# Kernel optimization log

Measured on AMD Instinct MI355X. Metric: run time of the kernel, lower is better.

The kernel has to match this reference:

```python
import jax, jax.numpy as jnp
import numpy as np

B, C, H, W, S = 32, 512, 32, 32, 4
HW = H * W
OUT = HW // S  # conv1/conv2 out channels = 256
EPS = 1e-5


def setup_inputs() -> dict:
    key = jax.random.key(0)
    ks = jax.random.split(key, 8)
    d = {}
    d["x"] = jax.random.normal(ks[0], (B, C, H, W), jnp.float32)
    # conv1 / bn1 (operate on x_flat with 'channels' = h*w)
    d["w1"] = jax.random.normal(ks[1], (OUT, HW), jnp.float32) * 0.02
    d["b1"] = jnp.zeros((OUT,), jnp.float32)
    d["g1"] = jnp.ones((OUT,), jnp.float32)
    d["be1"] = jnp.zeros((OUT,), jnp.float32)
    d["m1"] = jax.random.normal(ks[2], (OUT,), jnp.float32) * 0.01
    d["v1"] = jnp.ones((OUT,), jnp.float32)
    # conv2 / bn2
    d["w2"] = jax.random.normal(ks[3], (OUT, HW), jnp.float32) * 0.02
    d["b2"] = jnp.zeros((OUT,), jnp.float32)
    d["g2"] = jnp.ones((OUT,), jnp.float32)
    d["be2"] = jnp.zeros((OUT,), jnp.float32)
    d["m2"] = jax.random.normal(ks[4], (OUT,), jnp.float32) * 0.01
    d["v2"] = jnp.ones((OUT,), jnp.float32)
    # conv3 / bn3 (1x1 conv on the real channel dim c)
    d["w3"] = jax.random.normal(ks[5], (C, C), jnp.float32) * 0.02
    d["b3"] = jnp.zeros((C,), jnp.float32)
    d["g3"] = jnp.ones((C,), jnp.float32)
    d["be3"] = jnp.zeros((C,), jnp.float32)
    d["m3"] = jax.random.normal(ks[6], (C,), jnp.float32) * 0.01
    d["v3"] = jnp.ones((C,), jnp.float32)
    # conv4: 1x1 conv mapping 1+2c channels -> 1
    d["w4"] = jax.random.normal(ks[7], (1 + 2 * C,), jnp.float32) * 0.02
    d["b4"] = jnp.zeros((), jnp.float32)
    return d


def _bn1d(t, g, be, m, v):
    # t: [b, o, c]; BatchNorm (eval mode) over channel axis 1
    scale = g / jnp.sqrt(v + EPS)
    return (t - m[:, None]) * scale[:, None] + be[:, None]


def reference(x, w1, b1, g1, be1, m1, v1,
              w2, b2, g2, be2, m2, v2,
              w3, b3, g3, be3, m3, v3,
              w4, b4):
    b, c, h, w = x.shape
    # x_flat: [b, h*w, c] -- conv1/conv2 are 1x1 convs over 'channels' = h*w
    xf = x.reshape(b, c, h * w).transpose(0, 2, 1)
    theta = jax.nn.relu(_bn1d(jnp.einsum('oq,bqc->boc', w1, xf) + b1[:, None],
                              g1, be1, m1, v1))  # [b, OUT, c]
    phi = jax.nn.relu(_bn1d(jnp.einsum('oq,bqc->boc', w2, xf) + b2[:, None],
                            g2, be2, m2, v2))    # [b, OUT, c]
    # per-batch conv2d-as-matmul loop collapses to one batched GEMM:
    # affinity[b, i, j] = sum_k phi[b, k, i] * theta[b, k, j]
    aff = jnp.einsum('bki,bkj->bij', phi, theta)  # [b, c, c]
    # x_embed: 1x1 conv + BN + ReLU + global average pool -> [b, c]
    scale3 = g3 / jnp.sqrt(v3 + EPS)
    xe = jnp.einsum('oc,bchw->bohw', w3, x) + b3[:, None, None]
    xe = jax.nn.relu((xe - m3[:, None, None]) * scale3[:, None, None]
                     + be3[:, None, None])
    xe = xe.mean(axis=(2, 3))  # [b, c]
    # conv4 over y = cat([x_embed, affinity_a, affinity_b], dim=1):
    # affinity_a[b,i,0,p] = aff[b,i,p]; affinity_b[b,i,0,p] = aff[b,p,i]
    logits = (w4[0] * xe
              + jnp.einsum('i,bip->bp', w4[1:1 + c], aff)
              + jnp.einsum('i,bpi->bp', w4[1 + c:], aff)
              + b4)
    a = jax.nn.sigmoid(logits)  # [b, c]
    return x * a[:, :, None, None]
```

## Files before the change

kernel.cpp:

```cpp
#include <hip/hip_runtime.h>
#include <math.h>

#define BB   32
#define CC   512
#define HWW  1024
#define OUTC 256
#define EPSV 1e-5f

typedef __attribute__((ext_vector_type(8))) short bfrag;
typedef __attribute__((ext_vector_type(4))) float f32x4;

__device__ inline unsigned short f2bf(float x){
  unsigned int uu = __float_as_uint(x);
  uu += 0x7fff + ((uu >> 16) & 1);
  return (unsigned short)(uu >> 16);
}
__device__ inline float bf2f(unsigned short h){
  return __uint_as_float(((unsigned int)h) << 16);
}

#define ASYNC16(g, l) \
  __builtin_amdgcn_global_load_lds((const __attribute__((address_space(1))) unsigned int*)(g), \
                                   (__attribute__((address_space(3))) unsigned int*)(l), 16, 0, 0)


__global__ __launch_bounds__(256) void prep(
    const float* __restrict__ x,
    const float* __restrict__ w1, const float* __restrict__ w2,
    const float* __restrict__ w3,
    unsigned short* __restrict__ Xhi, unsigned short* __restrict__ Xlo,
    unsigned short* __restrict__ XThi,
    unsigned short* __restrict__ Whi, unsigned short* __restrict__ Wlo,
    unsigned short* __restrict__ W3hi)
{
  if (blockIdx.z == 32) {
    int worker = (blockIdx.y * 16 + blockIdx.x) * 256 + threadIdx.x;
    for (int i = worker; i < 786432; i += 32768) {
      if (i < 524288) {
        float v = (i < 262144) ? w1[i] : w2[i - 262144];
        unsigned short h = f2bf(v);
        Whi[i] = h;
        Wlo[i] = f2bf(v - bf2f(h));
      } else {
        int j = i - 524288;
        W3hi[j] = f2bf(w3[j]);
      }
    }
    return;
  }
  __shared__ float T[64][65];
  const int b = blockIdx.z, c0 = blockIdx.y * 64, p0 = blockIdx.x * 64;
  const int tid = threadIdx.x, tr = tid >> 4, tc4 = (tid & 15) * 4;
  const float* xb = x + (size_t)b * 512 * 1024;
#pragma unroll
  for (int r = 0; r < 4; ++r) {
    int c = c0 + tr + r * 16;
    float4 v = *(const float4*)(xb + (size_t)c * 1024 + p0 + tc4);
    T[tr + r * 16][tc4 + 0] = v.x; T[tr + r * 16][tc4 + 1] = v.y;
    T[tr + r * 16][tc4 + 2] = v.z; T[tr + r * 16][tc4 + 3] = v.w;
    ushort4 h, l;
    h.x = f2bf(v.x); l.x = f2bf(v.x - bf2f(h.x));
    h.y = f2bf(v.y); l.y = f2bf(v.y - bf2f(h.y));
    h.z = f2bf(v.z); l.z = f2bf(v.z - bf2f(h.z));
    h.w = f2bf(v.w); l.w = f2bf(v.w - bf2f(h.w));
    size_t idx = (size_t)b * 524288 + (size_t)c * 1024 + p0 + tc4;
    *(ushort4*)(Xhi + idx) = h;
    *(ushort4*)(Xlo + idx) = l;
  }
  __syncthreads();
#pragma unroll
  for (int r = 0; r < 4; ++r) {
    int pl = tr + r * 16;
    ushort4 h;
    h.x = f2bf(T[tc4 + 0][pl]); h.y = f2bf(T[tc4 + 1][pl]);
    h.z = f2bf(T[tc4 + 2][pl]); h.w = f2bf(T[tc4 + 3][pl]);
    *(ushort4*)(XThi + (size_t)b * 524288 + (size_t)(p0 + pl) * 512 + c0 + tc4) = h;
  }
}

__global__ __launch_bounds__(256) void g1_mfma(
    const unsigned short* __restrict__ Xhi, const unsigned short* __restrict__ Xlo,
    const unsigned short* __restrict__ Whi, const unsigned short* __restrict__ Wlo,
    const float* __restrict__ b1p, const float* __restrict__ g1p,
    const float* __restrict__ be1p, const float* __restrict__ m1p, const float* __restrict__ v1p,
    const float* __restrict__ b2p, const float* __restrict__ g2p,
    const float* __restrict__ be2p, const float* __restrict__ m2p, const float* __restrict__ v2p,
    const float* __restrict__ w4,
    float* __restrict__ P2, float* __restrict__ u, float* __restrict__ t)
{
  __shared__ unsigned short sAh[4096], sAl[4096], sBh[4096], sBl[4096];
  const int f    = blockIdx.x;
  const int xcd  = f & 7;
  const int n0   = ((f >> 3) & 3) * 128;
  const int g    = ((f >> 5) << 3) | xcd;
  const int b    = g >> 2;
  const int c0   = (g & 3) * 128;
  const int tid  = threadIdx.x;
  const int wave = tid >> 6, lane = tid & 63;
  const int lr = lane >> 2;
  const int lcs = ((lane & 3) ^ (lr & 3)) * 8;
  const int wm = wave & 1, wn = wave >> 1;
  const int fr = lane & 15, fq = lane >> 4;
  const int fsw = (fq ^ (fr & 3)) * 8;

  const unsigned short* gb; unsigned short* lb;
  if (wave == 0)      { gb = Xhi + (size_t)b * 524288 + (size_t)c0 * 1024; lb = sAh; }
  else if (wave == 1) { gb = Xlo + (size_t)b * 524288 + (size_t)c0 * 1024; lb = sAl; }
  else if (wave == 2) { gb = Whi + (size_t)n0 * 1024; lb = sBh; }
  else                { gb = Wlo + (size_t)n0 * 1024; lb = sBl; }
  gb += (size_t)lr * 1024 + lcs;

  f32x4 acc[4][4];
  const f32x4 zz = {0.f, 0.f, 0.f, 0.f};
#pragma unroll
  for (int i = 0; i < 4; ++i)
#pragma unroll
    for (int j = 0; j < 4; ++j) acc[i][j] = zz;

  for (int kq = 0; kq < 1024; kq += 32) {
#pragma unroll
    for (int inst = 0; inst < 8; ++inst)
      ASYNC16(gb + (size_t)inst * 16 * 1024 + kq, lb + inst * 512);
    __syncthreads();
    bfrag ah[4], al[4], bh[4], bl[4];
#pragma unroll
    for (int i = 0; i < 4; ++i) {
      int off = (wm * 64 + i * 16 + fr) * 32 + fsw;
      ah[i] = *(const bfrag*)&sAh[off];
      al[i] = *(const bfrag*)&sAl[off];
    }
#pragma unroll
    for (int j = 0; j < 4; ++j) {
      int off = (wn * 64 + j * 16 + fr) * 32 + fsw;
      bh[j] = *(const bfrag*)&sBh[off];
      bl[j] = *(const bfrag*)&sBl[off];
    }
#pragma unroll
    for (int i = 0; i < 4; ++i)
#pragma unroll
      for (int j = 0; j < 4; ++j) {
        acc[i][j] = __builtin_amdgcn_mfma_f32_16x16x32_bf16(ah[i], bh[j], acc[i][j], 0, 0, 0);
        acc[i][j] = __builtin_amdgcn_mfma_f32_16x16x32_bf16(ah[i], bl[j], acc[i][j], 0, 0, 0);
        acc[i][j] = __builtin_amdgcn_mfma_f32_16x16x32_bf16(al[i], bh[j], acc[i][j], 0, 0, 0);
      }
    __syncthreads();
  }

  const float *bias, *gg, *bes, *mm, *vv_; int cof;
  if (n0 < 256) { bias = b1p; gg = g1p; bes = be1p; mm = m1p; vv_ = v1p; cof = 0; }
  else          { bias = b2p; gg = g2p; bes = be2p; mm = m2p; vv_ = v2p; cof = 256; }
  const float* wsel = (n0 < 256) ? (w4 + 513) : (w4 + 1);
  float* dsel = (n0 < 256) ? (t + b * 256) : (u + b * 256);
  const int cobase = ((n0 < 256) ? n0 : n0 - 256) + wn * 64;
  float wt[4][4];
#pragma unroll
  for (int i = 0; i < 4; ++i)
#pragma unroll
    for (int r = 0; r < 4; ++r)
      wt[i][r] = wsel[c0 + wm * 64 + i * 16 + fq * 4 + r];

#pragma unroll
  for (int j = 0; j < 4; ++j) {
    int co = n0 + wn * 64 + j * 16 + fr;
    int q = co - cof;
    float s  = gg[q] * rsqrtf(vv_[q] + EPSV);
    float sh = (bias[q] - mm[q]) * s + bes[q];
    float psum = 0.f;
#pragma unroll
    for (int i = 0; i < 4; ++i) {
      int crow = c0 + wm * 64 + i * 16 + fq * 4;
      float* dst = P2 + ((size_t)b * 512 + crow) * 512 + co;
#pragma unroll
      for (int r = 0; r < 4; ++r) {
        float val = fmaxf(acc[i][j][r] * s + sh, 0.f);
        dst[(size_t)r * 512] = val;
        psum += wt[i][r] * val;
      }
    }
    psum += __shfl_xor(psum, 16);
    psum += __shfl_xor(psum, 32);
    if (fq == 0) atomicAdd(&dsel[cobase + j * 16 + fr], psum);
  }
}

__global__ __launch_bounds__(256) void g2_mfma(
    const unsigned short* __restrict__ W3hi, const unsigned short* __restrict__ XThi,
    const float* __restrict__ b3p, const float* __restrict__ g3p,
    const float* __restrict__ be3p, const float* __restrict__ m3p, const float* __restrict__ v3p,
    float* __restrict__ xe_acc)
{
  __shared__ unsigned short sA[4096], sB[4096];
  const int b  = blockIdx.z;
  const int n0 = blockIdx.x * 128;
  const int m0 = blockIdx.y * 128;
  const int tid = threadIdx.x;
  const int wave = tid >> 6, lane = tid & 63;
  const int lr = lane >> 2;
  const int lcs = ((lane & 3) ^ (lr & 3)) * 8;
  const int wm = wave & 1, wn = wave >> 1;
  const int fr = lane & 15, fq = lane >> 4;
  const int fsw = (fq ^ (fr & 3)) * 8;

  const unsigned short* gb; unsigned short* lb;
  if (wave < 2) { gb = W3hi + (size_t)(m0 + wave * 64) * 512; lb = sA + wave * 2048; }
  else { gb = XThi + (size_t)b * 524288 + (size_t)(n0 + (wave - 2) * 64) * 512; lb = sB + (wave - 2) * 2048; }
  gb += (size_t)lr * 512 + lcs;

  f32x4 acc[4][4];
  const f32x4 zz = {0.f, 0.f, 0.f, 0.f};
#pragma unroll
  for (int i = 0; i < 4; ++i)
#pragma unroll
    for (int j = 0; j < 4; ++j) acc[i][j] = zz;

  for (int kq = 0; kq < 512; kq += 32) {
#pragma unroll
    for (int inst = 0; inst < 4; ++inst)
      ASYNC16(gb + (size_t)inst * 16 * 512 + kq, lb + inst * 512);
    __syncthreads();
    bfrag af[4], bf[4];
#pragma unroll
    for (int i = 0; i < 4; ++i)
      af[i] = *(const bfrag*)&sA[(wm * 64 + i * 16 + fr) * 32 + fsw];
#pragma unroll
    for (int j = 0; j < 4; ++j)
      bf[j] = *(const bfrag*)&sB[(wn * 64 + j * 16 + fr) * 32 + fsw];
#pragma unroll
    for (int i = 0; i < 4; ++i)
#pragma unroll
      for (int j = 0; j < 4; ++j)
        acc[i][j] = __builtin_amdgcn_mfma_f32_16x16x32_bf16(af[i], bf[j], acc[i][j], 0, 0, 0);
    __syncthreads();
  }

#pragma unroll
  for (int i = 0; i < 4; ++i) {
#pragma unroll
    for (int r = 0; r < 4; ++r) {
      int o = m0 + wm * 64 + i * 16 + fq * 4 + r;
      float s  = g3p[o] * rsqrtf(v3p[o] + EPSV);
      float sh = (b3p[o] - m3p[o]) * s + be3p[o];
      float v = fmaxf(acc[i][0][r] * s + sh, 0.f) + fmaxf(acc[i][1][r] * s + sh, 0.f)
              + fmaxf(acc[i][2][r] * s + sh, 0.f) + fmaxf(acc[i][3][r] * s + sh, 0.f);
      v += __shfl_xor(v, 1); v += __shfl_xor(v, 2);
      v += __shfl_xor(v, 4); v += __shfl_xor(v, 8);
      if (fr == 0) atomicAdd(&xe_acc[b * 512 + o], v);
    }
  }
}

__global__ __launch_bounds__(256) void k4_gate_out(
    const float* __restrict__ P2, const float* __restrict__ u,
    const float* __restrict__ t, const float* __restrict__ xe_acc,
    const float* __restrict__ w4, const float* __restrict__ b4,
    const float* __restrict__ x, float* __restrict__ out)
{
  __shared__ float us[256], ts[256];
  const int b = blockIdx.x;
  us[threadIdx.x] = u[b * 256 + threadIdx.x];
  ts[threadIdx.x] = t[b * 256 + threadIdx.x];
  __syncthreads();
  const int wave = threadIdx.x >> 6, lane = threadIdx.x & 63;
  const int p = blockIdx.y * 4 + wave;
  const float* row = P2 + ((size_t)b * 512 + p) * 512;
  float4 th = *(const float4*)&row[lane * 4];
  float4 ph = *(const float4*)&row[256 + lane * 4];
  int ki = lane * 4;
  float rs = th.x * us[ki] + th.y * us[ki + 1] + th.z * us[ki + 2] + th.w * us[ki + 3]
           + ph.x * ts[ki] + ph.y * ts[ki + 1] + ph.z * ts[ki + 2] + ph.w * ts[ki + 3];
  rs += __shfl_xor(rs, 1);  rs += __shfl_xor(rs, 2);  rs += __shfl_xor(rs, 4);
  rs += __shfl_xor(rs, 8);  rs += __shfl_xor(rs, 16); rs += __shfl_xor(rs, 32);
  float xe = xe_acc[b * 512 + p] * (1.f / 1024.f);
  float logit = w4[0] * xe + rs + b4[0];
  float a = 1.f / (1.f + expf(-logit));
  const float4* xr = (const float4*)(x + ((size_t)b * 512 + p) * 1024);
  float4* orow = (float4*)(out + ((size_t)b * 512 + p) * 1024);
#pragma unroll
  for (int r2 = 0; r2 < 4; ++r2) {
    float4 xv = xr[lane + r2 * 64];
    float4 ov; ov.x = xv.x * a; ov.y = xv.y * a; ov.z = xv.z * a; ov.w = xv.w * a;
    orow[lane + r2 * 64] = ov;
  }
}

__global__ __launch_bounds__(256) void k1_theta_phi(
    const float* __restrict__ x,
    const float* __restrict__ w1, const float* __restrict__ b1,
    const float* __restrict__ g1, const float* __restrict__ be1,
    const float* __restrict__ m1, const float* __restrict__ v1,
    const float* __restrict__ w2, const float* __restrict__ b2,
    const float* __restrict__ g2, const float* __restrict__ be2,
    const float* __restrict__ m2, const float* __restrict__ v2,
    float* __restrict__ P)
{
  __shared__ __align__(16) float Ws[32][68];
  __shared__ __align__(16) float Xs[32][68];
  const int b  = blockIdx.z;
  const int o0 = blockIdx.y * 64;
  const int c0 = blockIdx.x * 64;
  const int tid = threadIdx.x;
  const int tx = tid & 15, ty = tid >> 4;
  const float* __restrict__ Wbase = (o0 < OUTC) ? (w1 + (size_t)o0 * HWW)
                                                : (w2 + (size_t)(o0 - OUTC) * HWW);
  const float* __restrict__ xb = x + (size_t)b * CC * HWW;
  float acc[4][4] = {{0.f}};
  for (int k0 = 0; k0 < HWW; k0 += 32) {
#pragma unroll
    for (int r = 0; r < 2; ++r) {
      int id  = tid + (r << 8);
      int row = id >> 3;
      int cg  = (id & 7) << 2;
      float4 wv = *(const float4*)(Wbase + (size_t)row * HWW + k0 + cg);
      Ws[cg+0][row] = wv.x; Ws[cg+1][row] = wv.y; Ws[cg+2][row] = wv.z; Ws[cg+3][row] = wv.w;
      float4 xv = *(const float4*)(xb + (size_t)(c0 + row) * HWW + k0 + cg);
      Xs[cg+0][row] = xv.x; Xs[cg+1][row] = xv.y; Xs[cg+2][row] = xv.z; Xs[cg+3][row] = xv.w;
    }
    __syncthreads();
#pragma unroll
    for (int k = 0; k < 32; ++k) {
      float4 av = *(const float4*)&Ws[k][ty * 4];
      float4 bv = *(const float4*)&Xs[k][tx * 4];
      acc[0][0] += av.x*bv.x; acc[0][1] += av.x*bv.y; acc[0][2] += av.x*bv.z; acc[0][3] += av.x*bv.w;
      acc[1][0] += av.y*bv.x; acc[1][1] += av.y*bv.y; acc[1][2] += av.y*bv.z; acc[1][3] += av.y*bv.w;
      acc[2][0] += av.z*bv.x; acc[2][1] += av.z*bv.y; acc[2][2] += av.z*bv.z; acc[2][3] += av.z*bv.w;
      acc[3][0] += av.w*bv.x; acc[3][1] += av.w*bv.y; acc[3][2] += av.w*bv.z; acc[3][3] += av.w*bv.w;
    }
    __syncthreads();
  }
  const float *bias, *g, *be, *m, *v; int ob;
  if (o0 < OUTC) { bias = b1; g = g1; be = be1; m = m1; v = v1; ob = o0; }
  else           { bias = b2; g = g2; be = be2; m = m2; v = v2; ob = o0 - OUTC; }
#pragma unroll
  for (int i = 0; i < 4; ++i) {
    int oi = ob + ty * 4 + i;
    float sc = g[oi] * rsqrtf(v[oi] + EPSV);
    float sh = be[oi] - m[oi] * sc;
    float bb = bias[oi];
    float4 ov;
    ov.x = fmaxf((acc[i][0] + bb) * sc + sh, 0.f);
    ov.y = fmaxf((acc[i][1] + bb) * sc + sh, 0.f);
    ov.z = fmaxf((acc[i][2] + bb) * sc + sh, 0.f);
    ov.w = fmaxf((acc[i][3] + bb) * sc + sh, 0.f);
    int oo = o0 + ty * 4 + i;
    *(float4*)(P + ((size_t)b * 512 + oo) * 512 + c0 + tx * 4) = ov;
  }
}

__global__ __launch_bounds__(256) void k2_xe(
    const float* __restrict__ x, const float* __restrict__ w3,
    const float* __restrict__ b3, const float* __restrict__ g3,
    const float* __restrict__ be3, const float* __restrict__ m3,
    const float* __restrict__ v3, float* __restrict__ xe_acc)
{
  __shared__ __align__(16) float As[32][68];
  __shared__ __align__(16) float Bs[32][68];
  const int b  = blockIdx.z;
  const int o0 = blockIdx.y * 64;
  const int p0 = blockIdx.x * 64;
  const int tid = threadIdx.x;
  const int tx = tid & 15, ty = tid >> 4;
  const float* __restrict__ xb = x + (size_t)b * CC * HWW;
  float acc[4][4] = {{0.f}};
  for (int ck = 0; ck < CC; ck += 32) {
#pragma unroll
// ... 59 lines not shown
  for (int off = 32; off > 0; off >>= 1) {
    su += __shfl_down(su, off);
    st += __shfl_down(st, off);
  }
  if (lane == 0) { u[b * OUTC + k] = su; t[b * OUTC + k] = st; }
}

__global__ __launch_bounds__(256) void k4_gate(
    const float* __restrict__ P, const float* __restrict__ u,
    const float* __restrict__ t, const float* __restrict__ xe_acc,
    const float* __restrict__ w4, const float* __restrict__ b4,
    float* __restrict__ amul)
{
  __shared__ float us[256], ts[256];
  const int b = blockIdx.x;
  const int p = blockIdx.y * 256 + threadIdx.x;
  us[threadIdx.x] = u[b * OUTC + threadIdx.x];
  ts[threadIdx.x] = t[b * OUTC + threadIdx.x];
  __syncthreads();
  const float* __restrict__ theta = P + (size_t)b * 512 * 512;
  const float* __restrict__ phi   = theta + 256 * 512;
  float r = 0.f, s = 0.f;
#pragma unroll 8
  for (int k = 0; k < OUTC; ++k) {
    r += us[k] * theta[(size_t)k * 512 + p];
    s += ts[k] * phi[(size_t)k * 512 + p];
  }
  float xe = xe_acc[b * CC + p] * (1.0f / 1024.0f);
  float logit = w4[0] * xe + r + s + b4[0];
  amul[b * CC + p] = 1.0f / (1.0f + expf(-logit));
}

__global__ __launch_bounds__(256) void k5_out(
    const float* __restrict__ x, const float* __restrict__ amul,
    float* __restrict__ out)
{
  int i = blockIdx.x * 256 + threadIdx.x;
  float4 xv = ((const float4*)x)[i];
  float a = amul[i >> 8];
  float4 ov; ov.x = xv.x * a; ov.y = xv.y * a; ov.z = xv.z * a; ov.w = xv.w * a;
  ((float4*)out)[i] = ov;
}

extern "C" void kernel_launch(void* const* d_in, const int* in_sizes, int n_in,
                              void* d_out, int out_size, void* d_ws, size_t ws_size,
                              hipStream_t stream)
{
  (void)in_sizes; (void)n_in; (void)out_size;
  const float* x   = (const float*)d_in[0];
  const float* w1  = (const float*)d_in[1];
  const float* b1  = (const float*)d_in[2];
  const float* g1  = (const float*)d_in[3];
  const float* be1 = (const float*)d_in[4];
  const float* m1  = (const float*)d_in[5];
  const float* v1  = (const float*)d_in[6];
  const float* w2  = (const float*)d_in[7];
  const float* b2  = (const float*)d_in[8];
  const float* g2  = (const float*)d_in[9];
  const float* be2 = (const float*)d_in[10];
  const float* m2  = (const float*)d_in[11];
  const float* v2  = (const float*)d_in[12];
  const float* w3  = (const float*)d_in[13];
  const float* b3  = (const float*)d_in[14];
  const float* g3  = (const float*)d_in[15];
  const float* be3 = (const float*)d_in[16];
  const float* m3  = (const float*)d_in[17];
  const float* v3  = (const float*)d_in[18];
  const float* w4  = (const float*)d_in[19];
  const float* b4  = (const float*)d_in[20];
  float* out = (float*)d_out;

  if (ws_size >= 136970240ull) {
    float* P2     = (float*)d_ws;
    float* xe_acc = P2 + 8388608;
    float* u      = P2 + 8404992;
    float* t      = P2 + 8413184;
    unsigned short* Xhi  = (unsigned short*)((char*)d_ws + 33685504);
    unsigned short* Xlo  = Xhi + 16777216;
    unsigned short* XThi = Xlo + 16777216;
    unsigned short* Whi  = XThi + 16777216;
    unsigned short* Wlo  = Whi + 524288;
    unsigned short* W3hi = Wlo + 524288;

    hipMemsetAsync(xe_acc, 0, 32768 * sizeof(float), stream);

    prep<<<dim3(16, 8, 33), 256, 0, stream>>>(x, w1, w2, w3, Xhi, Xlo, XThi,
                                              Whi, Wlo, W3hi);
    g1_mfma<<<dim3(512), 256, 0, stream>>>(Xhi, Xlo, Whi, Wlo,
        b1, g1, be1, m1, v1, b2, g2, be2, m2, v2, w4, P2, u, t);
    g2_mfma<<<dim3(8, 4, 32), 256, 0, stream>>>(W3hi, XThi, b3, g3, be3, m3, v3, xe_acc);
    k4_gate_out<<<dim3(32, 128), 256, 0, stream>>>(P2, u, t, xe_acc, w4, b4, x, out);
  } else {
    float* P      = (float*)d_ws;
    float* xe_acc = P + (size_t)BB * 512 * 512;
    float* u      = xe_acc + BB * CC;
    float* t      = u + BB * OUTC;
    float* amul   = t + BB * OUTC;

    hipMemsetAsync(xe_acc, 0, (size_t)BB * CC * sizeof(float), stream);

    dim3 blk(256);
    k1_theta_phi<<<dim3(8, 8, BB), blk, 0, stream>>>(x, w1, b1, g1, be1, m1, v1,
                                                     w2, b2, g2, be2, m2, v2, P);
    k2_xe<<<dim3(16, 8, BB), blk, 0, stream>>>(x, w3, b3, g3, be3, m3, v3, xe_acc);
    k3_ut<<<dim3(BB, 64), blk, 0, stream>>>(P, w4, u, t);
    k4_gate<<<dim3(BB, 2), blk, 0, stream>>>(P, u, t, xe_acc, w4, b4, amul);
    k5_out<<<dim3((BB * CC * HWW / 4) / 256), blk, 0, stream>>>(x, amul, out);
  }
}
```

Baseline: 291.8 us.

## Fuse both GEMM kernels into one launch and fold accumulator zeroing into prep

The theta/phi GEMM and the x_embed GEMM now run as two block ranges of a single kernel, so the two run concurrently instead of back to back. The theta/phi tile is narrowed from 128 to 64 output columns, which doubles its block count to fill more CUs. The separate memset of the xe/u/t accumulators is replaced by zeroing inside the prep kernel's weight-conversion blocks. In exchange, the narrower tiles reload the same X tiles from memory twice as often, and the shared-memory size is set by the larger of the two paths.

```diff
diff --git a/kernel.cpp b/kernel.cpp
--- a/kernel.cpp
+++ b/kernel.cpp
@@ -31,10 +31,12 @@
     unsigned short* __restrict__ Xhi, unsigned short* __restrict__ Xlo,
     unsigned short* __restrict__ XThi,
     unsigned short* __restrict__ Whi, unsigned short* __restrict__ Wlo,
-    unsigned short* __restrict__ W3hi)
+    unsigned short* __restrict__ W3hi,
+    float* __restrict__ accz)
 {
   if (blockIdx.z == 32) {
     int worker = (blockIdx.y * 16 + blockIdx.x) * 256 + threadIdx.x;
+    accz[worker] = 0.f;
     for (int i = worker; i < 786432; i += 32768) {
       if (i < 524288) {
         float v = (i < 262144) ? w1[i] : w2[i - 262144];
@@ -78,173 +80,170 @@
   }
 }
 
-__global__ __launch_bounds__(256) void g1_mfma(
+__global__ __launch_bounds__(256) void gemm_fused(
     const unsigned short* __restrict__ Xhi, const unsigned short* __restrict__ Xlo,
     const unsigned short* __restrict__ Whi, const unsigned short* __restrict__ Wlo,
+    const unsigned short* __restrict__ W3hi, const unsigned short* __restrict__ XThi,
     const float* __restrict__ b1p, const float* __restrict__ g1p,
     const float* __restrict__ be1p, const float* __restrict__ m1p, const float* __restrict__ v1p,
     const float* __restrict__ b2p, const float* __restrict__ g2p,
     const float* __restrict__ be2p, const float* __restrict__ m2p, const float* __restrict__ v2p,
+    const float* __restrict__ b3p, const float* __restrict__ g3p,
+    const float* __restrict__ be3p, const float* __restrict__ m3p, const float* __restrict__ v3p,
     const float* __restrict__ w4,
-    float* __restrict__ P2, float* __restrict__ u, float* __restrict__ t)
-{
-  __shared__ unsigned short sAh[4096], sAl[4096], sBh[4096], sBl[4096];
-  const int f    = blockIdx.x;
-  const int xcd  = f & 7;
-  const int n0   = ((f >> 3) & 3) * 128;
-  const int g    = ((f >> 5) << 3) | xcd;
-  const int b    = g >> 2;
-  const int c0   = (g & 3) * 128;
+    float* __restrict__ P2, float* __restrict__ u, float* __restrict__ t,
+    float* __restrict__ xe_acc)
+{
+  __shared__ unsigned short smem[12288];
+  const int fid  = blockIdx.x;
   const int tid  = threadIdx.x;
   const int wave = tid >> 6, lane = tid & 63;
   const int lr = lane >> 2;
   const int lcs = ((lane & 3) ^ (lr & 3)) * 8;
-  const int wm = wave & 1, wn = wave >> 1;
   const int fr = lane & 15, fq = lane >> 4;
   const int fsw = (fq ^ (fr & 3)) * 8;
 
-  const unsigned short* gb; unsigned short* lb;
-  if (wave == 0)      { gb = Xhi + (size_t)b * 524288 + (size_t)c0 * 1024; lb = sAh; }
-  else if (wave == 1) { gb = Xlo + (size_t)b * 524288 + (size_t)c0 * 1024; lb = sAl; }
-  else if (wave == 2) { gb = Whi + (size_t)n0 * 1024; lb = sBh; }
-  else                { gb = Wlo + (size_t)n0 * 1024; lb = sBl; }
-  gb += (size_t)lr * 1024 + lcs;
-
-  f32x4 acc[4][4];
-  const f32x4 zz = {0.f, 0.f, 0.f, 0.f};
-#pragma unroll
-  for (int i = 0; i < 4; ++i)
-#pragma unroll
-    for (int j = 0; j < 4; ++j) acc[i][j] = zz;
-
-  for (int kq = 0; kq < 1024; kq += 32) {
-#pragma unroll
-    for (int inst = 0; inst < 8; ++inst)
-      ASYNC16(gb + (size_t)inst * 16 * 1024 + kq, lb + inst * 512);
-    __syncthreads();
-    bfrag ah[4], al[4], bh[4], bl[4];
+  if (fid < 1024) {
+    unsigned short* sAh = smem;
+    unsigned short* sAl = smem + 4096;
+    unsigned short* sBh = smem + 8192;
+    unsigned short* sBl = smem + 10240;
+    const int xcd = fid & 7;
+    const int n0  = ((fid >> 3) & 7) * 64;
+    const int bc  = ((fid >> 6) << 3) | xcd;
+    const int b   = bc >> 2;
+    const int c0  = (bc & 3) * 128;
+    const int wm = wave & 1, wn = wave >> 1;
+
+    const unsigned short* gb; unsigned short* lb; int ninst;
+    if (wave == 0)      { gb = Xhi + (size_t)b * 524288 + (size_t)c0 * 1024; lb = sAh; ninst = 8; }
+    else if (wave == 1) { gb = Xlo + (size_t)b * 524288 + (size_t)c0 * 1024; lb = sAl; ninst = 8; }
+    else if (wave == 2) { gb = Whi + (size_t)n0 * 1024; lb = sBh; ninst = 4; }
+    else                { gb = Wlo + (size_t)n0 * 1024; lb = sBl; ninst = 4; }
+    gb += (size_t)lr * 1024 + lcs;
+
+    f32x4 acc[4][2];
+    const f32x4 zz = {0.f, 0.f, 0.f, 0.f};
+#pragma unroll
+    for (int i = 0; i < 4; ++i) { acc[i][0] = zz; acc[i][1] = zz; }
+
+    for (int kq = 0; kq < 1024; kq += 32) {
+      for (int inst = 0; inst < ninst; ++inst)
+        ASYNC16(gb + (size_t)inst * 16 * 1024 + kq, lb + inst * 512);
+      __syncthreads();
+      bfrag ah[4], al[4], bh[2], bl[2];
+#pragma unroll
+      for (int i = 0; i < 4; ++i) {
+        int off = (wm * 64 + i * 16 + fr) * 32 + fsw;
+        ah[i] = *(const bfrag*)&sAh[off];
+        al[i] = *(const bfrag*)&sAl[off];
+      }
+#pragma unroll
+      for (int j = 0; j < 2; ++j) {
+        int off = (wn * 32 + j * 16 + fr) * 32 + fsw;
+        bh[j] = *(const bfrag*)&sBh[off];
+        bl[j] = *(const bfrag*)&sBl[off];
+      }
+#pragma unroll
+      for (int i = 0; i < 4; ++i)
+#pragma unroll
+        for (int j = 0; j < 2; ++j) {
+          acc[i][j] = __builtin_amdgcn_mfma_f32_16x16x32_bf16(ah[i], bh[j], acc[i][j], 0, 0, 0);
+          acc[i][j] = __builtin_amdgcn_mfma_f32_16x16x32_bf16(ah[i], bl[j], acc[i][j], 0, 0, 0);
+          acc[i][j] = __builtin_amdgcn_mfma_f32_16x16x32_bf16(al[i], bh[j], acc[i][j], 0, 0, 0);
+        }
+      __syncthreads();
+    }
+
+    const float *bias, *gg, *bes, *mm, *vv_; int cof;
+    if (n0 < 256) { bias = b1p; gg = g1p; bes = be1p; mm = m1p; vv_ = v1p; cof = 0; }
+    else          { bias = b2p; gg = g2p; bes = be2p; mm = m2p; vv_ = v2p; cof = 256; }
+    const float* wsel = (n0 < 256) ? (w4 + 513) : (w4 + 1);
+    float* dsel = (n0 < 256) ? (t + b * 256) : (u + b * 256);
+    const int cobase = (n0 - cof) + wn * 32;
+    float wt[4][4];
+#pragma unroll
+    for (int i = 0; i < 4; ++i)
+#pragma unroll
+      for (int r = 0; r < 4; ++r)
+        wt[i][r] = wsel[c0 + wm * 64 + i * 16 + fq * 4 + r];
+
+#pragma unroll
+    for (int j = 0; j < 2; ++j) {
+      int co = n0 + wn * 32 + j * 16 + fr;
+      int q = co - cof;
+      float s  = gg[q] * rsqrtf(vv_[q] + EPSV);
+      float sh = (bias[q] - mm[q]) * s + bes[q];
+      float psum = 0.f;
+#pragma unroll
+      for (int i = 0; i < 4; ++i) {
+        int crow = c0 + wm * 64 + i * 16 + fq * 4;
+        float* dst = P2 + ((size_t)b * 512 + crow) * 512 + co;
+#pragma unroll
+        for (int r = 0; r < 4; ++r) {
+          float val = fmaxf(acc[i][j][r] * s + sh, 0.f);
+          dst[(size_t)r * 512] = val;
+          psum += wt[i][r] * val;
+        }
+      }
+      psum += __shfl_xor(psum, 16);
+      psum += __shfl_xor(psum, 32);
+      if (fq == 0) atomicAdd(&dsel[cobase + j * 16 + fr], psum);
+    }
+  } else {
+    unsigned short* sA = smem;
+    unsigned short* sB = smem + 4096;
+    const int h  = fid - 1024;
+    const int n0 = (h & 7) * 128;
+    const int m0 = ((h >> 3) & 3) * 128;
+    const int b  = h >> 5;
+    const int wm = wave & 1, wn = wave >> 1;
+
+    const unsigned short* gb; unsigned short* lb;
+    if (wave < 2) { gb = W3hi + (size_t)(m0 + wave * 64) * 512; lb = sA + wave * 2048; }
+    else { gb = XThi + (size_t)b * 524288 + (size_t)(n0 + (wave - 2) * 64) * 512; lb = sB + (wave - 2) * 2048; }
+    gb += (size_t)lr * 512 + lcs;
+
+    f32x4 acc[4][4];
+    const f32x4 zz = {0.f, 0.f, 0.f, 0.f};
+#pragma unroll
+    for (int i = 0; i < 4; ++i)
+#pragma unroll
+      for (int j = 0; j < 4; ++j) acc[i][j] = zz;
+
+    for (int kq = 0; kq < 512; kq += 32) {
+#pragma unroll
+      for (int inst = 0; inst < 4; ++inst)
+        ASYNC16(gb + (size_t)inst * 16 * 512 + kq, lb + inst * 512);
+      __syncthreads();
+      bfrag af[4], bf[4];
+#pragma unroll
+      for (int i = 0; i < 4; ++i)
+        af[i] = *(const bfrag*)&sA[(wm * 64 + i * 16 + fr) * 32 + fsw];
+#pragma unroll
+      for (int j = 0; j < 4; ++j)
+        bf[j] = *(const bfrag*)&sB[(wn * 64 + j * 16 + fr) * 32 + fsw];
+#pragma unroll
+      for (int i = 0; i < 4; ++i)
+#pragma unroll
+        for (int j = 0; j < 4; ++j)
+          acc[i][j] = __builtin_amdgcn_mfma_f32_16x16x32_bf16(af[i], bf[j], acc[i][j], 0, 0, 0);
+      __syncthreads();
+    }
+
 #pragma unroll
     for (int i = 0; i < 4; ++i) {
-      int off = (wm * 64 + i * 16 + fr) * 32 + fsw;
-      ah[i] = *(const bfrag*)&sAh[off];
-      al[i] = *(const bfrag*)&sAl[off];
-    }
-#pragma unroll
-    for (int j = 0; j < 4; ++j) {
-      int off = (wn * 64 + j * 16 + fr) * 32 + fsw;
-      bh[j] = *(const bfrag*)&sBh[off];
-      bl[j] = *(const bfrag*)&sBl[off];
-    }
-#pragma unroll
-    for (int i = 0; i < 4; ++i)
-#pragma unroll
-      for (int j = 0; j < 4; ++j) {
-        acc[i][j] = __builtin_amdgcn_mfma_f32_16x16x32_bf16(ah[i], bh[j], acc[i][j], 0, 0, 0);
-        acc[i][j] = __builtin_amdgcn_mfma_f32_16x16x32_bf16(ah[i], bl[j], acc[i][j], 0, 0, 0);
-        acc[i][j] = __builtin_amdgcn_mfma_f32_16x16x32_bf16(al[i], bh[j], acc[i][j], 0, 0, 0);
+#pragma unroll
+      for (int r = 0; r < 4; ++r) {
+        int o = m0 + wm * 64 + i * 16 + fq * 4 + r;
+        float s  = g3p[o] * rsqrtf(v3p[o] + EPSV);
+        float sh = (b3p[o] - m3p[o]) * s + be3p[o];
+        float v = fmaxf(acc[i][0][r] * s + sh, 0.f) + fmaxf(acc[i][1][r] * s + sh, 0.f)
+                + fmaxf(acc[i][2][r] * s + sh, 0.f) + fmaxf(acc[i][3][r] * s + sh, 0.f);
+        v += __shfl_xor(v, 1); v += __shfl_xor(v, 2);
+        v += __shfl_xor(v, 4); v += __shfl_xor(v, 8);
+        if (fr == 0) atomicAdd(&xe_acc[b * 512 + o], v);
       }
-    __syncthreads();
-  }
-
-  const float *bias, *gg, *bes, *mm, *vv_; int cof;
-  if (n0 < 256) { bias = b1p; gg = g1p; bes = be1p; mm = m1p; vv_ = v1p; cof = 0; }
-  else          { bias = b2p; gg = g2p; bes = be2p; mm = m2p; vv_ = v2p; cof = 256; }
-  const float* wsel = (n0 < 256) ? (w4 + 513) : (w4 + 1);
-  float* dsel = (n0 < 256) ? (t + b * 256) : (u + b * 256);
-  const int cobase = ((n0 < 256) ? n0 : n0 - 256) + wn * 64;
-  float wt[4][4];
-#pragma unroll
-  for (int i = 0; i < 4; ++i)
-#pragma unroll
-    for (int r = 0; r < 4; ++r)
-      wt[i][r] = wsel[c0 + wm * 64 + i * 16 + fq * 4 + r];
-
-#pragma unroll
-  for (int j = 0; j < 4; ++j) {
-    int co = n0 + wn * 64 + j * 16 + fr;
-    int q = co - cof;
-    float s  = gg[q] * rsqrtf(vv_[q] + EPSV);
-    float sh = (bias[q] - mm[q]) * s + bes[q];
-    float psum = 0.f;
-#pragma unroll
-    for (int i = 0; i < 4; ++i) {
-      int crow = c0 + wm * 64 + i * 16 + fq * 4;
-      float* dst = P2 + ((size_t)b * 512 + crow) * 512 + co;
-#pragma unroll
-      for (int r = 0; r < 4; ++r) {
-        float val = fmaxf(acc[i][j][r] * s + sh, 0.f);
-        dst[(size_t)r * 512] = val;
-        psum += wt[i][r] * val;
-      }
-    }
-    psum += __shfl_xor(psum, 16);
-    psum += __shfl_xor(psum, 32);
-    if (fq == 0) atomicAdd(&dsel[cobase + j * 16 + fr], psum);
-  }
-}
-
-__global__ __launch_bounds__(256) void g2_mfma(
-    const unsigned short* __restrict__ W3hi, const unsigned short* __restrict__ XThi,
-    const float* __restrict__ b3p, const float* __restrict__ g3p,
-    const float* __restrict__ be3p, const float* __restrict__ m3p, const float* __restrict__ v3p,
-    float* __restrict__ xe_acc)
-{
-  __shared__ unsigned short sA[4096], sB[4096];
-  const int b  = blockIdx.z;
-  const int n0 = blockIdx.x * 128;
-  const int m0 = blockIdx.y * 128;
-  const int tid = threadIdx.x;
-  const int wave = tid >> 6, lane = tid & 63;
-  const int lr = lane >> 2;
-  const int lcs = ((lane & 3) ^ (lr & 3)) * 8;
-  const int wm = wave & 1, wn = wave >> 1;
-  const int fr = lane & 15, fq = lane >> 4;
-  const int fsw = (fq ^ (fr & 3)) * 8;
-
-  const unsigned short* gb; unsigned short* lb;
-  if (wave < 2) { gb = W3hi + (size_t)(m0 + wave * 64) * 512; lb = sA + wave * 2048; }
-  else { gb = XThi + (size_t)b * 524288 + (size_t)(n0 + (wave - 2) * 64) * 512; lb = sB + (wave - 2) * 2048; }
-  gb += (size_t)lr * 512 + lcs;
-
-  f32x4 acc[4][4];
-  const f32x4 zz = {0.f, 0.f, 0.f, 0.f};
-#pragma unroll
-  for (int i = 0; i < 4; ++i)
-#pragma unroll
-    for (int j = 0; j < 4; ++j) acc[i][j] = zz;
-
-  for (int kq = 0; kq < 512; kq += 32) {
-#pragma unroll
-    for (int inst = 0; inst < 4; ++inst)
-      ASYNC16(gb + (size_t)inst * 16 * 512 + kq, lb + inst * 512);
-    __syncthreads();
-    bfrag af[4], bf[4];
-#pragma unroll
-    for (int i = 0; i < 4; ++i)
-      af[i] = *(const bfrag*)&sA[(wm * 64 + i * 16 + fr) * 32 + fsw];
-#pragma unroll
-    for (int j = 0; j < 4; ++j)
-      bf[j] = *(const bfrag*)&sB[(wn * 64 + j * 16 + fr) * 32 + fsw];
-#pragma unroll
-    for (int i = 0; i < 4; ++i)
-#pragma unroll
-      for (int j = 0; j < 4; ++j)
-        acc[i][j] = __builtin_amdgcn_mfma_f32_16x16x32_bf16(af[i], bf[j], acc[i][j], 0, 0, 0);
-    __syncthreads();
-  }
-
-#pragma unroll
-  for (int i = 0; i < 4; ++i) {
-#pragma unroll
-    for (int r = 0; r < 4; ++r) {
-      int o = m0 + wm * 64 + i * 16 + fq * 4 + r;
-      float s  = g3p[o] * rsqrtf(v3p[o] + EPSV);
-      float sh = (b3p[o] - m3p[o]) * s + be3p[o];
-      float v = fmaxf(acc[i][0][r] * s + sh, 0.f) + fmaxf(acc[i][1][r] * s + sh, 0.f)
-              + fmaxf(acc[i][2][r] * s + sh, 0.f) + fmaxf(acc[i][3][r] * s + sh, 0.f);
-      v += __shfl_xor(v, 1); v += __shfl_xor(v, 2);
-      v += __shfl_xor(v, 4); v += __shfl_xor(v, 8);
-      if (fr == 0) atomicAdd(&xe_acc[b * 512 + o], v);
     }
   }
 }
@@ -505,13 +504,11 @@
     unsigned short* Wlo  = Whi + 524288;
     unsigned short* W3hi = Wlo + 524288;
 
-    hipMemsetAsync(xe_acc, 0, 32768 * sizeof(float), stream);
-
     prep<<<dim3(16, 8, 33), 256, 0, stream>>>(x, w1, w2, w3, Xhi, Xlo, XThi,
-                                              Whi, Wlo, W3hi);
-    g1_mfma<<<dim3(512), 256, 0, stream>>>(Xhi, Xlo, Whi, Wlo,
-        b1, g1, be1, m1, v1, b2, g2, be2, m2, v2, w4, P2, u, t);
-    g2_mfma<<<dim3(8, 4, 32), 256, 0, stream>>>(W3hi, XThi, b3, g3, be3, m3, v3, xe_acc);
+                                              Whi, Wlo, W3hi, xe_acc);
+    gemm_fused<<<dim3(2048), 256, 0, stream>>>(Xhi, Xlo, Whi, Wlo, W3hi, XThi,
+        b1, g1, be1, m1, v1, b2, g2, be2, m2, v2, b3, g3, be3, m3, v3,
+        w4, P2, u, t, xe_acc);
     k4_gate_out<<<dim3(32, 128), 256, 0, stream>>>(P2, u, t, xe_acc, w4, b4, x, out);
   } else {
     float* P      = (float*)d_ws;
```

Measured after the change: 289.1 us. Within noise of the previous version (-0.9%).

## Merge conv1/conv2 and conv3 GEMMs into one interleaved launch, drop memset

Applied to the files above, without the earlier changes.

The two MFMA GEMM kernels become one launch whose blocks are interleaved, one theta/phi tile for every two x_embed tiles, so both GEMMs can share the GPU at once and the tail of the first no longer idles it. Zeroing of the xe_acc/u/t accumulators moves from a separate memset into the weight-conversion blocks of prep, removing one stream operation. The gate/output kernel now handles four channel rows per wave with a quarter of the blocks. In exchange, every block of the fused kernel reserves the larger 32KB shared buffer, which can lower occupancy for the conv3 tiles.

```diff
diff --git a/kernel.cpp b/kernel.cpp
--- a/kernel.cpp
+++ b/kernel.cpp
@@ -31,10 +31,12 @@
     unsigned short* __restrict__ Xhi, unsigned short* __restrict__ Xlo,
     unsigned short* __restrict__ XThi,
     unsigned short* __restrict__ Whi, unsigned short* __restrict__ Wlo,
-    unsigned short* __restrict__ W3hi)
+    unsigned short* __restrict__ W3hi,
+    float* __restrict__ accz)
 {
   if (blockIdx.z == 32) {
     int worker = (blockIdx.y * 16 + blockIdx.x) * 256 + threadIdx.x;
+    accz[worker] = 0.f;
     for (int i = worker; i < 786432; i += 32768) {
       if (i < 524288) {
         float v = (i < 262144) ? w1[i] : w2[i - 262144];
@@ -78,23 +80,22 @@
   }
 }
 
-__global__ __launch_bounds__(256) void g1_mfma(
+__global__ __launch_bounds__(256) void gemm_fused(
     const unsigned short* __restrict__ Xhi, const unsigned short* __restrict__ Xlo,
     const unsigned short* __restrict__ Whi, const unsigned short* __restrict__ Wlo,
+    const unsigned short* __restrict__ W3hi, const unsigned short* __restrict__ XThi,
     const float* __restrict__ b1p, const float* __restrict__ g1p,
     const float* __restrict__ be1p, const float* __restrict__ m1p, const float* __restrict__ v1p,
     const float* __restrict__ b2p, const float* __restrict__ g2p,
     const float* __restrict__ be2p, const float* __restrict__ m2p, const float* __restrict__ v2p,
+    const float* __restrict__ b3p, const float* __restrict__ g3p,
+    const float* __restrict__ be3p, const float* __restrict__ m3p, const float* __restrict__ v3p,
     const float* __restrict__ w4,
-    float* __restrict__ P2, float* __restrict__ u, float* __restrict__ t)
-{
-  __shared__ unsigned short sAh[4096], sAl[4096], sBh[4096], sBl[4096];
-  const int f    = blockIdx.x;
-  const int xcd  = f & 7;
-  const int n0   = ((f >> 3) & 3) * 128;
-  const int g    = ((f >> 5) << 3) | xcd;
-  const int b    = g >> 2;
-  const int c0   = (g & 3) * 128;
+    float* __restrict__ P2, float* __restrict__ u, float* __restrict__ t,
+    float* __restrict__ xe_acc)
+{
+  __shared__ unsigned short smem[16384];
+  const int fid  = blockIdx.x;
   const int tid  = threadIdx.x;
   const int wave = tid >> 6, lane = tid & 63;
   const int lr = lane >> 2;
@@ -103,148 +104,149 @@
   const int fr = lane & 15, fq = lane >> 4;
   const int fsw = (fq ^ (fr & 3)) * 8;
 
-  const unsigned short* gb; unsigned short* lb;
-  if (wave == 0)      { gb = Xhi + (size_t)b * 524288 + (size_t)c0 * 1024; lb = sAh; }
-  else if (wave == 1) { gb = Xlo + (size_t)b * 524288 + (size_t)c0 * 1024; lb = sAl; }
-  else if (wave == 2) { gb = Whi + (size_t)n0 * 1024; lb = sBh; }
-  else                { gb = Wlo + (size_t)n0 * 1024; lb = sBl; }
-  gb += (size_t)lr * 1024 + lcs;
-
-  f32x4 acc[4][4];
-  const f32x4 zz = {0.f, 0.f, 0.f, 0.f};
-#pragma unroll
-  for (int i = 0; i < 4; ++i)
-#pragma unroll
-    for (int j = 0; j < 4; ++j) acc[i][j] = zz;
-
-  for (int kq = 0; kq < 1024; kq += 32) {
-#pragma unroll
-    for (int inst = 0; inst < 8; ++inst)
-      ASYNC16(gb + (size_t)inst * 16 * 1024 + kq, lb + inst * 512);
-    __syncthreads();
-    bfrag ah[4], al[4], bh[4], bl[4];
+  if (fid % 3 == 0) {
+    unsigned short* sAh = smem;
+    unsigned short* sAl = smem + 4096;
+    unsigned short* sBh = smem + 8192;
+    unsigned short* sBl = smem + 12288;
+    const int m  = fid / 3;
+    const int n0 = (m >> 7) * 128;
+    const int g  = m & 127;
+    const int b  = g >> 2;
+    const int c0 = (g & 3) * 128;
+
+    const unsigned short* gb; unsigned short* lb;
+    if (wave == 0)      { gb = Xhi + (size_t)b * 524288 + (size_t)c0 * 1024; lb = sAh; }
+    else if (wave == 1) { gb = Xlo + (size_t)b * 524288 + (size_t)c0 * 1024; lb = sAl; }
+    else if (wave == 2) { gb = Whi + (size_t)n0 * 1024; lb = sBh; }
+    else                { gb = Wlo + (size_t)n0 * 1024; lb = sBl; }
+    gb += (size_t)lr * 1024 + lcs;
+
+    f32x4 acc[4][4];
+    const f32x4 zz = {0.f, 0.f, 0.f, 0.f};
+#pragma unroll
+    for (int i = 0; i < 4; ++i)
+#pragma unroll
+      for (int j = 0; j < 4; ++j) acc[i][j] = zz;
+
+    for (int kq = 0; kq < 1024; kq += 32) {
+#pragma unroll
+      for (int inst = 0; inst < 8; ++inst)
+        ASYNC16(gb + (size_t)inst * 16 * 1024 + kq, lb + inst * 512);
+      __syncthreads();
+      bfrag ah[4], al[4], bh[4], bl[4];
+#pragma unroll
+      for (int i = 0; i < 4; ++i) {
+        int off = (wm * 64 + i * 16 + fr) * 32 + fsw;
+        ah[i] = *(const bfrag*)&sAh[off];
+        al[i] = *(const bfrag*)&sAl[off];
+      }
+#pragma unroll
+      for (int j = 0; j < 4; ++j) {
+        int off = (wn * 64 + j * 16 + fr) * 32 + fsw;
+        bh[j] = *(const bfrag*)&sBh[off];
+        bl[j] = *(const bfrag*)&sBl[off];
+      }
+#pragma unroll
+      for (int i = 0; i < 4; ++i)
+#pragma unroll
+        for (int j = 0; j < 4; ++j) {
+          acc[i][j] = __builtin_amdgcn_mfma_f32_16x16x32_bf16(ah[i], bh[j], acc[i][j], 0, 0, 0);
+          acc[i][j] = __builtin_amdgcn_mfma_f32_16x16x32_bf16(ah[i], bl[j], acc[i][j], 0, 0, 0);
+          acc[i][j] = __builtin_amdgcn_mfma_f32_16x16x32_bf16(al[i], bh[j], acc[i][j], 0, 0, 0);
+        }
+      __syncthreads();
+    }
+
+    const float *bias, *gg, *bes, *mm, *vv_; int cof;
+    if (n0 < 256) { bias = b1p; gg = g1p; bes = be1p; mm = m1p; vv_ = v1p; cof = 0; }
+    else          { bias = b2p; gg = g2p; bes = be2p; mm = m2p; vv_ = v2p; cof = 256; }
+    const float* wsel = (n0 < 256) ? (w4 + 513) : (w4 + 1);
+    float* dsel = (n0 < 256) ? (t + b * 256) : (u + b * 256);
+    const int cobase = (n0 - cof) + wn * 64;
+    float wt[4][4];
+#pragma unroll
+    for (int i = 0; i < 4; ++i)
+#pragma unroll
+      for (int r = 0; r < 4; ++r)
+        wt[i][r] = wsel[c0 + wm * 64 + i * 16 + fq * 4 + r];
+
+#pragma unroll
+    for (int j = 0; j < 4; ++j) {
+      int co = n0 + wn * 64 + j * 16 + fr;
+      int q = co - cof;
+      float s  = gg[q] * rsqrtf(vv_[q] + EPSV);
+      float sh = (bias[q] - mm[q]) * s + bes[q];
+      float psum = 0.f;
+#pragma unroll
+      for (int i = 0; i < 4; ++i) {
+        int crow = c0 + wm * 64 + i * 16 + fq * 4;
+        float* dst = P2 + ((size_t)b * 512 + crow) * 512 + co;
+#pragma unroll
+        for (int r = 0; r < 4; ++r) {
+          float val = fmaxf(acc[i][j][r] * s + sh, 0.f);
+          dst[(size_t)r * 512] = val;
+          psum += wt[i][r] * val;
+        }
+      }
+      psum += __shfl_xor(psum, 16);
+      psum += __shfl_xor(psum, 32);
+      if (fq == 0) atomicAdd(&dsel[cobase + j * 16 + fr], psum);
+    }
+  } else {
+    unsigned short* sA = smem;
+    unsigned short* sB = smem + 4096;
+    const int h  = (fid / 3) * 2 + (fid % 3) - 1;
+    const int m0 = (h >> 8) * 128;
+    const int gg2 = h & 255;
+    const int b  = gg2 >> 3;
+    const int n0 = (gg2 & 7) * 128;
+
+    const unsigned short* gb; unsigned short* lb;
+    if (wave < 2) { gb = W3hi + (size_t)(m0 + wave * 64) * 512; lb = sA + wave * 2048; }
+    else { gb = XThi + (size_t)b * 524288 + (size_t)(n0 + (wave - 2) * 64) * 512; lb = sB + (wave - 2) * 2048; }
+    gb += (size_t)lr * 512 + lcs;
+
+    f32x4 acc[4][4];
+    const f32x4 zz = {0.f, 0.f, 0.f, 0.f};
+#pragma unroll
+    for (int i = 0; i < 4; ++i)
+#pragma unroll
+      for (int j = 0; j < 4; ++j) acc[i][j] = zz;
+
+    for (int kq = 0; kq < 512; kq += 32) {
+#pragma unroll
+      for (int inst = 0; inst < 4; ++inst)
+        ASYNC16(gb + (size_t)inst * 16 * 512 + kq, lb + inst * 512);
+      __syncthreads();
+      bfrag af[4], bf[4];
+#pragma unroll
+      for (int i = 0; i < 4; ++i)
+        af[i] = *(const bfrag*)&sA[(wm * 64 + i * 16 + fr) * 32 + fsw];
+#pragma unroll
+      for (int j = 0; j < 4; ++j)
+        bf[j] = *(const bfrag*)&sB[(wn * 64 + j * 16 + fr) * 32 + fsw];
+#pragma unroll
+      for (int i = 0; i < 4; ++i)
+#pragma unroll
+        for (int j = 0; j < 4; ++j)
+          acc[i][j] = __builtin_amdgcn_mfma_f32_16x16x32_bf16(af[i], bf[j], acc[i][j], 0, 0, 0);
+      __syncthreads();
+    }
+
 #pragma unroll
     for (int i = 0; i < 4; ++i) {
-      int off = (wm * 64 + i * 16 + fr) * 32 + fsw;
-      ah[i] = *(const bfrag*)&sAh[off];
-      al[i] = *(const bfrag*)&sAl[off];
-    }
-#pragma unroll
-    for (int j = 0; j < 4; ++j) {
-      int off = (wn * 64 + j * 16 + fr) * 32 + fsw;
-      bh[j] = *(const bfrag*)&sBh[off];
-      bl[j] = *(const bfrag*)&sBl[off];
-    }
-#pragma unroll
-    for (int i = 0; i < 4; ++i)
-#pragma unroll
-      for (int j = 0; j < 4; ++j) {
-        acc[i][j] = __builtin_amdgcn_mfma_f32_16x16x32_bf16(ah[i], bh[j], acc[i][j], 0, 0, 0);
-        acc[i][j] = __builtin_amdgcn_mfma_f32_16x16x32_bf16(ah[i], bl[j], acc[i][j], 0, 0, 0);
-        acc[i][j] = __builtin_amdgcn_mfma_f32_16x16x32_bf16(al[i], bh[j], acc[i][j], 0, 0, 0);
+#pragma unroll
+      for (int r = 0; r < 4; ++r) {
+        int o = m0 + wm * 64 + i * 16 + fq * 4 + r;
+        float s  = g3p[o] * rsqrtf(v3p[o] + EPSV);
+        float sh = (b3p[o] - m3p[o]) * s + be3p[o];
+        float v = fmaxf(acc[i][0][r] * s + sh, 0.f) + fmaxf(acc[i][1][r] * s + sh, 0.f)
+                + fmaxf(acc[i][2][r] * s + sh, 0.f) + fmaxf(acc[i][3][r] * s + sh, 0.f);
+        v += __shfl_xor(v, 1); v += __shfl_xor(v, 2);
+        v += __shfl_xor(v, 4); v += __shfl_xor(v, 8);
+        if (fr == 0) atomicAdd(&xe_acc[b * 512 + o], v);
       }
-    __syncthreads();
-  }
-
-  const float *bias, *gg, *bes, *mm, *vv_; int cof;
-  if (n0 < 256) { bias = b1p; gg = g1p; bes = be1p; mm = m1p; vv_ = v1p; cof = 0; }
-  else          { bias = b2p; gg = g2p; bes = be2p; mm = m2p; vv_ = v2p; cof = 256; }
-  const float* wsel = (n0 < 256) ? (w4 + 513) : (w4 + 1);
-  float* dsel = (n0 < 256) ? (t + b * 256) : (u + b * 256);
-  const int cobase = ((n0 < 256) ? n0 : n0 - 256) + wn * 64;
-  float wt[4][4];
-#pragma unroll
-  for (int i = 0; i < 4; ++i)
-#pragma unroll
-    for (int r = 0; r < 4; ++r)
-      wt[i][r] = wsel[c0 + wm * 64 + i * 16 + fq * 4 + r];
-
-#pragma unroll
-  for (int j = 0; j < 4; ++j) {
-    int co = n0 + wn * 64 + j * 16 + fr;
-    int q = co - cof;
-    float s  = gg[q] * rsqrtf(vv_[q] + EPSV);
-    float sh = (bias[q] - mm[q]) * s + bes[q];
-    float psum = 0.f;
-#pragma unroll
-    for (int i = 0; i < 4; ++i) {
-      int crow = c0 + wm * 64 + i * 16 + fq * 4;
-      float* dst = P2 + ((size_t)b * 512 + crow) * 512 + co;
-#pragma unroll
-      for (int r = 0; r < 4; ++r) {
-        float val = fmaxf(acc[i][j][r] * s + sh, 0.f);
-        dst[(size_t)r * 512] = val;
-        psum += wt[i][r] * val;
-      }
-    }
-    psum += __shfl_xor(psum, 16);
-    psum += __shfl_xor(psum, 32);
-    if (fq == 0) atomicAdd(&dsel[cobase + j * 16 + fr], psum);
-  }
-}
-
-__global__ __launch_bounds__(256) void g2_mfma(
-    const unsigned short* __restrict__ W3hi, const unsigned short* __restrict__ XThi,
-    const float* __restrict__ b3p, const float* __restrict__ g3p,
-    const float* __restrict__ be3p, const float* __restrict__ m3p, const float* __restrict__ v3p,
-    float* __restrict__ xe_acc)
-{
-  __shared__ unsigned short sA[4096], sB[4096];
-  const int b  = blockIdx.z;
-  const int n0 = blockIdx.x * 128;
-  const int m0 = blockIdx.y * 128;
-  const int tid = threadIdx.x;
-  const int wave = tid >> 6, lane = tid & 63;
-  const int lr = lane >> 2;
-  const int lcs = ((lane & 3) ^ (lr & 3)) * 8;
-  const int wm = wave & 1, wn = wave >> 1;
-  const int fr = lane & 15, fq = lane >> 4;
-  const int fsw = (fq ^ (fr & 3)) * 8;
-
-  const unsigned short* gb; unsigned short* lb;
-  if (wave < 2) { gb = W3hi + (size_t)(m0 + wave * 64) * 512; lb = sA + wave * 2048; }
-  else { gb = XThi + (size_t)b * 524288 + (size_t)(n0 + (wave - 2) * 64) * 512; lb = sB + (wave - 2) * 2048; }
-  gb += (size_t)lr * 512 + lcs;
-
-  f32x4 acc[4][4];
-  const f32x4 zz = {0.f, 0.f, 0.f, 0.f};
-#pragma unroll
-  for (int i = 0; i < 4; ++i)
-#pragma unroll
-    for (int j = 0; j < 4; ++j) acc[i][j] = zz;
-
-  for (int kq = 0; kq < 512; kq += 32) {
-#pragma unroll
-    for (int inst = 0; inst < 4; ++inst)
-      ASYNC16(gb + (size_t)inst * 16 * 512 + kq, lb + inst * 512);
-    __syncthreads();
-    bfrag af[4], bf[4];
-#pragma unroll
-    for (int i = 0; i < 4; ++i)
-      af[i] = *(const bfrag*)&sA[(wm * 64 + i * 16 + fr) * 32 + fsw];
-#pragma unroll
-    for (int j = 0; j < 4; ++j)
-      bf[j] = *(const bfrag*)&sB[(wn * 64 + j * 16 + fr) * 32 + fsw];
-#pragma unroll
-    for (int i = 0; i < 4; ++i)
-#pragma unroll
-      for (int j = 0; j < 4; ++j)
-        acc[i][j] = __builtin_amdgcn_mfma_f32_16x16x32_bf16(af[i], bf[j], acc[i][j], 0, 0, 0);
-    __syncthreads();
-  }
-
-#pragma unroll
-  for (int i = 0; i < 4; ++i) {
-#pragma unroll
-    for (int r = 0; r < 4; ++r) {
-      int o = m0 + wm * 64 + i * 16 + fq * 4 + r;
-      float s  = g3p[o] * rsqrtf(v3p[o] + EPSV);
-      float sh = (b3p[o] - m3p[o]) * s + be3p[o];
-      float v = fmaxf(acc[i][0][r] * s + sh, 0.f) + fmaxf(acc[i][1][r] * s + sh, 0.f)
-              + fmaxf(acc[i][2][r] * s + sh, 0.f) + fmaxf(acc[i][3][r] * s + sh, 0.f);
-      v += __shfl_xor(v, 1); v += __shfl_xor(v, 2);
-      v += __shfl_xor(v, 4); v += __shfl_xor(v, 8);
-      if (fr == 0) atomicAdd(&xe_acc[b * 512 + o], v);
     }
   }
 }
@@ -261,25 +263,29 @@
   ts[threadIdx.x] = t[b * 256 + threadIdx.x];
   __syncthreads();
   const int wave = threadIdx.x >> 6, lane = threadIdx.x & 63;
-  const int p = blockIdx.y * 4 + wave;
-  const float* row = P2 + ((size_t)b * 512 + p) * 512;
-  float4 th = *(const float4*)&row[lane * 4];
-  float4 ph = *(const float4*)&row[256 + lane * 4];
-  int ki = lane * 4;
-  float rs = th.x * us[ki] + th.y * us[ki + 1] + th.z * us[ki + 2] + th.w * us[ki + 3]
-           + ph.x * ts[ki] + ph.y * ts[ki + 1] + ph.z * ts[ki + 2] + ph.w * ts[ki + 3];
-  rs += __shfl_xor(rs, 1);  rs += __shfl_xor(rs, 2);  rs += __shfl_xor(rs, 4);
-  rs += __shfl_xor(rs, 8);  rs += __shfl_xor(rs, 16); rs += __shfl_xor(rs, 32);
-  float xe = xe_acc[b * 512 + p] * (1.f / 1024.f);
-  float logit = w4[0] * xe + rs + b4[0];
-  float a = 1.f / (1.f + expf(-logit));
-  const float4* xr = (const float4*)(x + ((size_t)b * 512 + p) * 1024);
-  float4* orow = (float4*)(out + ((size_t)b * 512 + p) * 1024);
-#pragma unroll
-  for (int r2 = 0; r2 < 4; ++r2) {
-    float4 xv = xr[lane + r2 * 64];
-    float4 ov; ov.x = xv.x * a; ov.y = xv.y * a; ov.z = xv.z * a; ov.w = xv.w * a;
-    orow[lane + r2 * 64] = ov;
+  const float w40 = w4[0], b40 = b4[0];
+#pragma unroll
+  for (int pp = 0; pp < 4; ++pp) {
+    const int p = blockIdx.y * 16 + wave * 4 + pp;
+    const float* row = P2 + ((size_t)b * 512 + p) * 512;
+    float4 th = *(const float4*)&row[lane * 4];
+    float4 ph = *(const float4*)&row[256 + lane * 4];
+    int ki = lane * 4;
+    float rs = th.x * us[ki] + th.y * us[ki + 1] + th.z * us[ki + 2] + th.w * us[ki + 3]
+             + ph.x * ts[ki] + ph.y * ts[ki + 1] + ph.z * ts[ki + 2] + ph.w * ts[ki + 3];
+    rs += __shfl_xor(rs, 1);  rs += __shfl_xor(rs, 2);  rs += __shfl_xor(rs, 4);
+    rs += __shfl_xor(rs, 8);  rs += __shfl_xor(rs, 16); rs += __shfl_xor(rs, 32);
+    float xe = xe_acc[b * 512 + p] * (1.f / 1024.f);
+    float logit = w40 * xe + rs + b40;
+    float a = 1.f / (1.f + expf(-logit));
+    const float4* xr = (const float4*)(x + ((size_t)b * 512 + p) * 1024);
+    float4* orow = (float4*)(out + ((size_t)b * 512 + p) * 1024);
+#pragma unroll
+    for (int r2 = 0; r2 < 4; ++r2) {
+      float4 xv = xr[lane + r2 * 64];
+      float4 ov; ov.x = xv.x * a; ov.y = xv.y * a; ov.z = xv.z * a; ov.w = xv.w * a;
+      orow[lane + r2 * 64] = ov;
+    }
   }
 }
 
@@ -505,14 +511,12 @@
     unsigned short* Wlo  = Whi + 524288;
     unsigned short* W3hi = Wlo + 524288;
 
-    hipMemsetAsync(xe_acc, 0, 32768 * sizeof(float), stream);
-
     prep<<<dim3(16, 8, 33), 256, 0, stream>>>(x, w1, w2, w3, Xhi, Xlo, XThi,
-                                              Whi, Wlo, W3hi);
-    g1_mfma<<<dim3(512), 256, 0, stream>>>(Xhi, Xlo, Whi, Wlo,
-        b1, g1, be1, m1, v1, b2, g2, be2, m2, v2, w4, P2, u, t);
-    g2_mfma<<<dim3(8, 4, 32), 256, 0, stream>>>(W3hi, XThi, b3, g3, be3, m3, v3, xe_acc);
-    k4_gate_out<<<dim3(32, 128), 256, 0, stream>>>(P2, u, t, xe_acc, w4, b4, x, out);
+                                              Whi, Wlo, W3hi, xe_acc);
+    gemm_fused<<<dim3(1536), 256, 0, stream>>>(Xhi, Xlo, Whi, Wlo, W3hi, XThi,
+        b1, g1, be1, m1, v1, b2, g2, be2, m2, v2, b3, g3, be3, m3, v3,
+        w4, P2, u, t, xe_acc);
+    k4_gate_out<<<dim3(32, 32), 256, 0, stream>>>(P2, u, t, xe_acc, w4, b4, x, out);
   } else {
     float* P      = (float*)d_ws;
     float* xe_acc = P + (size_t)BB * 512 * 512;
```

After: 320.4 us. 9.8% more time.
